# Optimization experiments

Hardware: AMD Instinct MI355X
Metric: run time of the kernel (lower is better)

## Reference

```python
import jax, jax.numpy as jnp
import numpy as np

VOCAB, D, MAX_LEN = 32000, 256, 128
BATCH, SEQ = 32, 128


def setup_inputs() -> dict:
    key = jax.random.key(0)
    ks = jax.random.split(key, 8)
    s = 1.0 / np.sqrt(D)  # torch nn.Linear default init scale
    X = jax.random.randint(ks[0], (BATCH, SEQ), 0, VOCAB)
    emb = jax.random.normal(ks[1], (VOCAB, D), dtype=jnp.float32)
    W_l = jax.random.uniform(ks[2], (D, D), minval=-s, maxval=s, dtype=jnp.float32)
    b_l = jax.random.uniform(ks[3], (D,), minval=-s, maxval=s, dtype=jnp.float32)
    W_r = jax.random.uniform(ks[4], (D, D), minval=-s, maxval=s, dtype=jnp.float32)
    b_r = jax.random.uniform(ks[5], (D,), minval=-s, maxval=s, dtype=jnp.float32)
    W_rn = jax.random.uniform(ks[6], (D, D), minval=-s, maxval=s, dtype=jnp.float32)
    b_rn = jax.random.uniform(ks[7], (D,), minval=-s, maxval=s, dtype=jnp.float32)
    return {"X": X, "emb": emb, "W_l": W_l, "b_l": b_l,
            "W_r": W_r, "b_r": b_r, "W_rn": W_rn, "b_rn": b_rn}


def reference(X, emb, W_l, b_l, W_r, b_r, W_rn, b_rn):
    X = X[:, :MAX_LEN]
    n = X.shape[1]
    Xe = emb[X]                               # (B, n, D) embedding lookup
    Xl = Xe @ W_l.T + b_l                     # (B, n, D)
    Xr = Xe @ W_r.T + b_r                     # (B, n, D)
    # pairwise: pair[b, i, j] = relu(Xl[b, j] + Xr[b, i])  -> (B, n, n, D)
    pair = jax.nn.relu(Xl[:, None, :, :] + Xr[:, :, None, :])
    # linear_rn then sum over (i, j); by linearity: sum(pair) @ W_rn.T + n^2 * b_rn
    pooled = pair.sum(axis=(1, 2))            # (B, D)
    return pooled @ W_rn.T + (n * n) * b_rn   # (B, D)
```

## Files before the change

### kernel.cpp

```cpp
#include <hip/hip_runtime.h>

#define D 256
#define S 128
#define B 32
#define DC 16

typedef __attribute__((ext_vector_type(8))) short bf16x8;
typedef __attribute__((ext_vector_type(4))) float f32x4;

__device__ __forceinline__ unsigned short f2bf(float f) {
    union { float f; unsigned u; } v; v.f = f;
    unsigned r = v.u + 0x7FFFu + ((v.u >> 16) & 1u);
    return (unsigned short)(r >> 16);
}

__device__ __forceinline__ float dot4(float4 a, float4 b) {
    return a.x * b.x + a.y * b.y + a.z * b.z + a.w * b.w;
}

__global__ __launch_bounds__(256) void k0_cast(
    const float* __restrict__ Wl, const float* __restrict__ Wr,
    unsigned short* __restrict__ Wb)
{
    const int idx = blockIdx.x * 256 + threadIdx.x;
    const int e = idx * 4;
    const int n = e >> 8, k = e & 255;
    const float* src = (n < 256) ? (Wl + (size_t)n * D + k)
                                 : (Wr + (size_t)(n - 256) * D + k);
    const float4 f = *(const float4*)src;
    ushort4 h;
    h.x = f2bf(f.x); h.y = f2bf(f.y); h.z = f2bf(f.z); h.w = f2bf(f.w);
    *(ushort4*)(Wb + (size_t)n * D + k) = h;
}

__global__ __launch_bounds__(256) void k1_mfma(
    const int* __restrict__ X, const float* __restrict__ emb,
    const unsigned short* __restrict__ Wb,
    const float* __restrict__ bl, const float* __restrict__ br,
    float* __restrict__ Xl, float* __restrict__ Xr)
{
    constexpr int LDA = 264;
    __shared__ unsigned short Asb[16 * LDA];

    const int tid = threadIdx.x;
    const int rowBase = (blockIdx.x >> 1) * 16;
    const int half = blockIdx.x & 1;

    {
        const int r = tid >> 4;
        const int c0 = (tid & 15) * 16;
        const int tok = X[rowBase + r];
        const float* src = emb + (size_t)tok * D + c0;
        unsigned short* dst = Asb + r * LDA + c0;
#pragma unroll
        for (int j4 = 0; j4 < 4; ++j4) {
            const float4 f = ((const float4*)src)[j4];
            ushort4 h;
            h.x = f2bf(f.x); h.y = f2bf(f.y); h.z = f2bf(f.z); h.w = f2bf(f.w);
            ((ushort4*)dst)[j4] = h;
        }
    }
    __syncthreads();

    const int w  = tid >> 6;
    const int l  = tid & 63;
    const int lm = l & 15;
    const int lq = l >> 4;

    const unsigned short* aptr = Asb + lm * LDA + lq * 8;
    const int n_base = half * 256 + w * 64;
    const unsigned short* bptr = Wb + (size_t)(n_base + lm) * D + lq * 8;

    f32x4 acc[4];
#pragma unroll
    for (int t = 0; t < 4; ++t) acc[t] = (f32x4){0.f, 0.f, 0.f, 0.f};

#pragma unroll
    for (int ks = 0; ks < 8; ++ks) {
        const bf16x8 a = *(const bf16x8*)(aptr + ks * 32);
#pragma unroll
        for (int t = 0; t < 4; ++t) {
            const bf16x8 b = *(const bf16x8*)(bptr + (size_t)t * 16 * D + ks * 32);
            acc[t] = __builtin_amdgcn_mfma_f32_16x16x32_bf16(a, b, acc[t], 0, 0, 0);
        }
    }

    const float* __restrict__ bias = half ? br : bl;
    float* __restrict__ Obase = half ? Xr : Xl;
#pragma unroll
    for (int t = 0; t < 4; ++t) {
        const int col = w * 64 + t * 16 + lm;
        const float bv = bias[col];
#pragma unroll
        for (int i = 0; i < 4; ++i) {
            const int row = rowBase + lq * 4 + i;
            Obase[(size_t)row * D + col] = acc[t][i] + bv;
        }
    }
}

__global__ __launch_bounds__(256) void k2_pairsum(
    const float* __restrict__ Xl, const float* __restrict__ Xr,
    float* __restrict__ pooled)
{
    __shared__ float lxl[S * DC];
    __shared__ float lxr[S * DC];
    __shared__ float red[256];

    const int b   = blockIdx.x >> 4;
    const int dc  = blockIdx.x & 15;
    const int tid = threadIdx.x;
    const int dl  = tid & (DC - 1);
    const int ig  = tid >> 4;

    const size_t base = (size_t)b * S * D + (size_t)dc * DC;
    {
        float4* lxl4 = (float4*)lxl;
        float4* lxr4 = (float4*)lxr;
#pragma unroll
        for (int t = 0; t < 2; ++t) {
            const int e4 = tid + t * 256;
            const int j = e4 >> 2, df = e4 & 3;
            const float4* pl = (const float4*)(Xl + base + (size_t)j * D);
            const float4* pr = (const float4*)(Xr + base + (size_t)j * D);
            lxl4[e4] = pl[df];
            lxr4[e4] = pr[df];
        }
    }
    __syncthreads();

    float xr[8];
    float sr = 0.f;
#pragma unroll
    for (int u = 0; u < 8; ++u) {
        xr[u] = lxr[(ig * 8 + u) * DC + dl];
        sr += xr[u];
    }

    float sabs = 0.f, sxl = 0.f;
#pragma unroll 4
    for (int j = 0; j < S; ++j) {
        const float x = lxl[j * DC + dl];
        sxl += x;
#pragma unroll
        for (int u = 0; u < 8; ++u)
            sabs += fabsf(x + xr[u]);
    }

    red[tid] = sabs + (float)S * sr;
    __syncthreads();

    if (tid < DC) {
        float tot = 0.f;
#pragma unroll
        for (int g = 0; g < 16; ++g) tot += red[g * DC + tid];
        pooled[(size_t)b * D + (size_t)dc * DC + tid] =
            0.5f * ((float)S * sxl + tot);
    }
}

__global__ __launch_bounds__(256) void k3_out(
    const float* __restrict__ pooled, const float* __restrict__ Wrn,
    const float* __restrict__ brn, float* __restrict__ out)
{
    __shared__ float lp[D];
    __shared__ float red[256];
    const int bb = blockIdx.x >> 3;
    const int dc = blockIdx.x & 7;
    const int tid = threadIdx.x;
    lp[tid] = pooled[(size_t)bb * D + tid];
    __syncthreads();

    const int dl = tid & 31;
    const int kg = tid >> 5;
    const int d = dc * 32 + dl;
    const float4* __restrict__ w4 = (const float4*)(Wrn + (size_t)d * D) + kg * 8;
    const float4* __restrict__ p4 = (const float4*)lp + kg * 8;
    float acc = 0.f;
#pragma unroll
    for (int f = 0; f < 8; ++f) acc += dot4(w4[f], p4[f]);

    red[tid] = acc;
    __syncthreads();
    if (tid < 32) {
        float s = 0.f;
#pragma unroll
        for (int g = 0; g < 8; ++g) s += red[g * 32 + tid];
        out[(size_t)bb * D + dc * 32 + tid] = s + (float)(S * S) * brn[dc * 32 + tid];
    }
}

extern "C" void kernel_launch(void* const* d_in, const int* in_sizes, int n_in,
                              void* d_out, int out_size, void* d_ws, size_t ws_size,
                              hipStream_t stream) {
    const int*   X   = (const int*)d_in[0];
    const float* emb = (const float*)d_in[1];
    const float* Wl  = (const float*)d_in[2];
    const float* bl  = (const float*)d_in[3];
    const float* Wr  = (const float*)d_in[4];
    const float* br  = (const float*)d_in[5];
    const float* Wrn = (const float*)d_in[6];
    const float* brn = (const float*)d_in[7];
    float* out = (float*)d_out;

    float* ws     = (float*)d_ws;
    float* Xl     = ws;
    float* Xr     = ws + (size_t)B * S * D;
    float* pooled = ws + 2 * (size_t)B * S * D;
    unsigned short* Wb = (unsigned short*)(pooled + B * D);

    k0_cast<<<128, 256, 0, stream>>>(Wl, Wr, Wb);
    k1_mfma<<<512, 256, 0, stream>>>(X, emb, Wb, bl, br, Xl, Xr);
    k2_pairsum<<<B * (D / DC), 256, 0, stream>>>(Xl, Xr, pooled);
    k3_out<<<B * 8, 256, 0, stream>>>(pooled, Wrn, brn, out);
}
```

Baseline: 112.7 us.

## Store Xl/Xr intermediates as bf16 and split pairsum accumulators

The projection kernel now writes Xl and Xr as bf16 instead of fp32, and the pairsum kernel reads bf16 and widens to fp32 in shared memory. This halves the intermediate traffic between the two kernels. Separately, the inner abs-sum now uses eight independent accumulators instead of one serial chain, which adds instruction-level parallelism. Storing intermediates at lower precision adds rounding error to the pooled sums.

```diff
diff --git a/kernel.cpp b/kernel.cpp
--- a/kernel.cpp
+++ b/kernel.cpp
@@ -13,7 +13,10 @@
     unsigned r = v.u + 0x7FFFu + ((v.u >> 16) & 1u);
     return (unsigned short)(r >> 16);
 }
-
+__device__ __forceinline__ float bf2f(unsigned short h) {
+    union { unsigned u; float f; } v; v.u = ((unsigned)h) << 16;
+    return v.f;
+}
 __device__ __forceinline__ float dot4(float4 a, float4 b) {
     return a.x * b.x + a.y * b.y + a.z * b.z + a.w * b.w;
 }
@@ -37,7 +40,7 @@
     const int* __restrict__ X, const float* __restrict__ emb,
     const unsigned short* __restrict__ Wb,
     const float* __restrict__ bl, const float* __restrict__ br,
-    float* __restrict__ Xl, float* __restrict__ Xr)
+    unsigned short* __restrict__ Xlb, unsigned short* __restrict__ Xrb)
 {
     constexpr int LDA = 264;
     __shared__ unsigned short Asb[16 * LDA];
@@ -86,7 +89,7 @@
     }
 
     const float* __restrict__ bias = half ? br : bl;
-    float* __restrict__ Obase = half ? Xr : Xl;
+    unsigned short* __restrict__ Obase = half ? Xrb : Xlb;
 #pragma unroll
     for (int t = 0; t < 4; ++t) {
         const int col = w * 64 + t * 16 + lm;
@@ -94,13 +97,13 @@
 #pragma unroll
         for (int i = 0; i < 4; ++i) {
             const int row = rowBase + lq * 4 + i;
-            Obase[(size_t)row * D + col] = acc[t][i] + bv;
+            Obase[(size_t)row * D + col] = f2bf(acc[t][i] + bv);
         }
     }
 }
 
 __global__ __launch_bounds__(256) void k2_pairsum(
-    const float* __restrict__ Xl, const float* __restrict__ Xr,
+    const unsigned short* __restrict__ Xlb, const unsigned short* __restrict__ Xrb,
     float* __restrict__ pooled)
 {
     __shared__ float lxl[S * DC];
@@ -115,16 +118,17 @@
 
     const size_t base = (size_t)b * S * D + (size_t)dc * DC;
     {
-        float4* lxl4 = (float4*)lxl;
-        float4* lxr4 = (float4*)lxr;
 #pragma unroll
         for (int t = 0; t < 2; ++t) {
-            const int e4 = tid + t * 256;
-            const int j = e4 >> 2, df = e4 & 3;
-            const float4* pl = (const float4*)(Xl + base + (size_t)j * D);
-            const float4* pr = (const float4*)(Xr + base + (size_t)j * D);
-            lxl4[e4] = pl[df];
-            lxr4[e4] = pr[df];
+            const int c4 = tid + t * 256;
+            const int j = c4 >> 2, df = c4 & 3;
+            const ushort4 hl = *(const ushort4*)(Xlb + base + (size_t)j * D + df * 4);
+            const ushort4 hr = *(const ushort4*)(Xrb + base + (size_t)j * D + df * 4);
+            float4 fl, fr;
+            fl.x = bf2f(hl.x); fl.y = bf2f(hl.y); fl.z = bf2f(hl.z); fl.w = bf2f(hl.w);
+            fr.x = bf2f(hr.x); fr.y = bf2f(hr.y); fr.z = bf2f(hr.z); fr.w = bf2f(hr.w);
+            *(float4*)(lxl + j * DC + df * 4) = fl;
+            *(float4*)(lxr + j * DC + df * 4) = fr;
         }
     }
     __syncthreads();
@@ -137,15 +141,20 @@
         sr += xr[u];
     }
 
-    float sabs = 0.f, sxl = 0.f;
+    float sa[8];
+#pragma unroll
+    for (int u = 0; u < 8; ++u) sa[u] = 0.f;
+    float sxl = 0.f;
 #pragma unroll 4
     for (int j = 0; j < S; ++j) {
         const float x = lxl[j * DC + dl];
         sxl += x;
 #pragma unroll
         for (int u = 0; u < 8; ++u)
-            sabs += fabsf(x + xr[u]);
-    }
+            sa[u] += fabsf(x + xr[u]);
+    }
+    float sabs = ((sa[0] + sa[1]) + (sa[2] + sa[3]))
+               + ((sa[4] + sa[5]) + (sa[6] + sa[7]));
 
     red[tid] = sabs + (float)S * sr;
     __syncthreads();
@@ -203,14 +212,14 @@
     const float* brn = (const float*)d_in[7];
     float* out = (float*)d_out;
 
-    float* ws     = (float*)d_ws;
-    float* Xl     = ws;
-    float* Xr     = ws + (size_t)B * S * D;
-    float* pooled = ws + 2 * (size_t)B * S * D;
+    const size_t NX = (size_t)B * S * D;
+    unsigned short* Xlb = (unsigned short*)d_ws;
+    unsigned short* Xrb = Xlb + NX;
+    float* pooled = (float*)(Xrb + NX);
     unsigned short* Wb = (unsigned short*)(pooled + B * D);
 
     k0_cast<<<128, 256, 0, stream>>>(Wl, Wr, Wb);
-    k1_mfma<<<512, 256, 0, stream>>>(X, emb, Wb, bl, br, Xl, Xr);
-    k2_pairsum<<<B * (D / DC), 256, 0, stream>>>(Xl, Xr, pooled);
+    k1_mfma<<<512, 256, 0, stream>>>(X, emb, Wb, bl, br, Xlb, Xrb);
+    k2_pairsum<<<B * (D / DC), 256, 0, stream>>>(Xlb, Xrb, pooled);
     k3_out<<<B * 8, 256, 0, stream>>>(pooled, Wrn, brn, out);
 }
```

Result: no change. 111.9 us (-0.7%).
